# Kernel tuning notes

Measured on AMD Instinct MI355X. Metric: run time of the kernel, lower is better.

## Reference

```python
import jax, jax.numpy as jnp
import numpy as np

B, D, OUT, K = 2048, 256, 256, 16


def setup_inputs() -> dict:
    key = jax.random.key(0)
    k1, k2, k3, k4 = jax.random.split(key, 4)
    x = jax.random.normal(k1, (B, D), dtype=jnp.float32)
    values = jax.random.uniform(k2, (OUT, D, K), dtype=jnp.float32, minval=-0.05, maxval=0.05)
    skip_w = jax.random.normal(k3, (OUT, D), dtype=jnp.float32) * (1.0 / np.sqrt(D).astype(np.float32))
    skip_b = jax.random.normal(k4, (OUT,), dtype=jnp.float32) * 0.01
    return {"x": x, "values": values, "skip_w": skip_w, "skip_b": skip_b}


def reference(x, values, skip_w, skip_b):
    # x: (B, D); values: (OUT, D, K); skip_w: (OUT, D); skip_b: (OUT,)
    num_knots = values.shape[-1]
    grid = jnp.linspace(-1.0, 1.0, num_knots)  # (K,)
    xc = jnp.clip(x, -1.0, 1.0)
    # torch.bucketize(x, grid) with right=False == searchsorted side='left'
    right = jnp.searchsorted(grid, xc, side='left')
    left = jnp.clip(right - 1, 0, num_knots - 2)  # (B, D)
    right = left + 1
    g0 = grid[left]
    g1 = grid[right]
    w = (xc - g0) / (g1 - g0 + 1e-12)  # (B, D)
    # Gather spline values per (sample, input-dim) knot bucket.
    vt = jnp.transpose(values, (1, 2, 0))  # (D, K, OUT)
    dim_idx = jnp.arange(xc.shape[1])[None, :]  # (1, D)
    v_left = vt[dim_idx, left]    # (B, D, OUT)
    v_right = vt[dim_idx, right]  # (B, D, OUT)
    # Linear interpolation + sum over input dims.
    y = jnp.sum((1.0 - w)[..., None] * v_left + w[..., None] * v_right, axis=1)  # (B, OUT)
    # Skip connection on the clamped input (torch reassigns x = clamp(x) first).
    return y + xc @ skip_w.T + skip_b
```

## Files before the change

kernel.cpp:

```cpp
#include <hip/hip_runtime.h>
#include <hip/hip_bf16.h>


namespace {
constexpr int Bsz  = 2048;
constexpr int Din  = 256;
constexpr int Dout = 256;
constexpr int Kn   = 16;
constexpr int KKNOT = Din * Kn;
constexpr int KB    = KKNOT / 32;
constexpr float INV_H = 7.5f;
constexpr float Hgrid = 2.0f / 15.0f;

constexpr int NSPLIT = 8;
constexpr int STK    = 8;
constexpr int SXS    = 36;
}

typedef __attribute__((ext_vector_type(8))) short shortx8;
typedef __attribute__((ext_vector_type(4))) float floatx4;

__device__ __forceinline__ unsigned int f2bf(float f) {
  __hip_bfloat16 h = __float2bfloat16(f);
  return (unsigned int)*reinterpret_cast<unsigned short*>(&h);
}
__device__ __forceinline__ float clamp1(float v) {
  return fminf(1.f, fmaxf(-1.f, v));
}
__device__ __forceinline__ unsigned int packbf(unsigned int e0, unsigned int e1) {
  return (e1 & 0xffff0000u) | (e0 >> 16);
}
__device__ __forceinline__ unsigned int rnd(float f) {
  return __float_as_uint(f) + 0x8000u;
}

__global__ __launch_bounds__(256) void kan_prep(
    const float* __restrict__ values, const float* __restrict__ skip_w,
    unsigned short* __restrict__ Wf) {
  const int tid = blockIdx.x * 256 + threadIdx.x;
  const int q  = tid & 3;
  const int n  = (tid >> 2) & 15;
  const int og = (tid >> 6) & 15;
  const int kb = tid >> 10;
  const int o  = og * 16 + n;
  const int k0 = kb * 32 + q * 8;
  const int d  = k0 >> 4;
  const float h0 = (float)(k0 & 15);
  const float sw = skip_w[o * Din + d];
  const float* src = values + (size_t)o * KKNOT + k0;
  const float4 v0 = *(const float4*)src;
  const float4 v1 = *(const float4*)(src + 4);
  float e[8] = {v0.x, v0.y, v0.z, v0.w, v1.x, v1.y, v1.z, v1.w};
  #pragma unroll
  for (int j = 0; j < 8; ++j)
    e[j] = fmaf(-1.f + (h0 + (float)j) * Hgrid, sw, e[j]);
  const size_t chunk = (size_t)kb * 1024 + og * 64 + q * 16 + n;
  *(uint4*)(Wf + chunk * 8) = make_uint4(
      f2bf(e[0]) | (f2bf(e[1]) << 16), f2bf(e[2]) | (f2bf(e[3]) << 16),
      f2bf(e[4]) | (f2bf(e[5]) << 16), f2bf(e[6]) | (f2bf(e[7]) << 16));
}

__global__ __launch_bounds__(256) void kan_gemm(
    const float* __restrict__ x, const unsigned short* __restrict__ Wf,
    float* __restrict__ part) {
  __shared__ float sx[32 * SXS];
  __shared__ __align__(16) unsigned short aLds[2][32 * 64];

  const int tid  = threadIdx.x;
  const int wave = tid >> 6, lane = tid & 63;
  const int ks   = blockIdx.x >> 6;
  const int mi   = blockIdx.x & 63;
  const int m0   = mi * 32;
  const int og0  = wave * 4;
  const int lrow = lane & 15, lq = lane >> 4;

  const int brow = tid >> 3;
  const int bseg = tid & 7;
  const int kbi  = bseg >> 2;
  const int dsel = (bseg >> 1) & 1;
  const float h0 = (float)((bseg & 1) * 8);

  const uint4* B = (const uint4*)Wf;

  floatx4 acc[2][4] = {};
  uint4 bb[2][8];

  const int kb0 = ks * 16;
  const int d0  = ks * 32;
  {
    const float4 v = *(const float4*)(x + (size_t)(m0 + brow) * Din + d0 + bseg * 4);
    *(float4*)&sx[brow * SXS + bseg * 4] = v;
  }
  __syncthreads();

  #pragma unroll
  for (int kk = 0; kk < 2; ++kk)
    #pragma unroll
    for (int j = 0; j < 4; ++j)
      bb[0][kk * 4 + j] = B[(size_t)(kb0 + kk) * 1024 + (og0 + j) * 64 + lane];
  {
    const float xv = sx[brow * SXS + 2 * kbi + dsel];
    const float t  = (clamp1(xv) + 1.f) * INV_H;
    unsigned int e[8];
    #pragma unroll
    for (int h = 0; h < 8; ++h)
      e[h] = rnd(fmaxf(0.f, 1.f - fabsf(t - (h0 + (float)h))));
    *(uint4*)&aLds[0][brow * 64 + bseg * 8] =
        make_uint4(packbf(e[0], e[1]), packbf(e[2], e[3]),
                   packbf(e[4], e[5]), packbf(e[6], e[7]));
  }

  for (int s = 0; s < STK; ++s) {
    const int cur = s & 1, nxt = cur ^ 1;
    if (s + 1 < STK) {
      #pragma unroll
      for (int kk = 0; kk < 2; ++kk)
        #pragma unroll
        for (int j = 0; j < 4; ++j)
          bb[nxt][kk * 4 + j] =
              B[(size_t)(kb0 + 2 * (s + 1) + kk) * 1024 + (og0 + j) * 64 + lane];
    }
    __syncthreads();

    if (s + 1 < STK) {
      const float xv = sx[brow * SXS + 4 * (s + 1) + 2 * kbi + dsel];
      const float t  = (clamp1(xv) + 1.f) * INV_H;
      unsigned int e[8];
      #pragma unroll
      for (int h = 0; h < 8; ++h)
        e[h] = rnd(fmaxf(0.f, 1.f - fabsf(t - (h0 + (float)h))));
      *(uint4*)&aLds[nxt][brow * 64 + bseg * 8] =
          make_uint4(packbf(e[0], e[1]), packbf(e[2], e[3]),
                     packbf(e[4], e[5]), packbf(e[6], e[7]));
    }

    shortx8 af[2][2];
    #pragma unroll
    for (int i = 0; i < 2; ++i)
      #pragma unroll
      for (int kk = 0; kk < 2; ++kk)
        af[i][kk] = *(const shortx8*)&aLds[cur][(16 * i + lrow) * 64 + kk * 32 + lq * 8];
    #pragma unroll
    for (int kk = 0; kk < 2; ++kk)
      #pragma unroll
      for (int j = 0; j < 4; ++j) {
        union { uint4 u; shortx8 s; } bc;
        bc.u = bb[cur][kk * 4 + j];
        #pragma unroll
        for (int i = 0; i < 2; ++i)
          acc[i][j] = __builtin_amdgcn_mfma_f32_16x16x32_bf16(af[i][kk], bc.s, acc[i][j], 0, 0, 0);
      }
  }

  float4* P4 = (float4*)part;
  const size_t sbase = ((size_t)mi * NSPLIT + ks) * 2048 + wave * 512;
  #pragma unroll
  for (int i = 0; i < 2; ++i)
    #pragma unroll
    for (int j = 0; j < 4; ++j)
      P4[sbase + (i * 4 + j) * 64 + lane] =
          make_float4(acc[i][j][0], acc[i][j][1], acc[i][j][2], acc[i][j][3]);
}

__global__ __launch_bounds__(256) void kan_reduce(
    const float* __restrict__ part, const float* __restrict__ skip_b,
    float* __restrict__ out) {
  const int mi = blockIdx.x >> 3;
  const int g  = ((blockIdx.x & 7) << 8) + threadIdx.x;
  const float4* Pm = (const float4*)part + (size_t)mi * NSPLIT * 2048;
  float4 a = Pm[g];
  #pragma unroll
  for (int sp = 1; sp < NSPLIT; ++sp) {
    const float4 b = Pm[sp * 2048 + g];
    a.x += b.x; a.y += b.y; a.z += b.z; a.w += b.w;
  }
  const int w  = g >> 9, qq = g & 511;
  const int ij = qq >> 6, ln = qq & 63;
  const int i  = ij >> 2, j = ij & 3;
  const int b0 = mi * 32 + 16 * i + ((ln >> 4) << 2);
  const int o  = w * 64 + 16 * j + (ln & 15);
  const float sb = skip_b[o];
  out[(size_t)(b0 + 0) * Dout + o] = a.x + sb;
  out[(size_t)(b0 + 1) * Dout + o] = a.y + sb;
  out[(size_t)(b0 + 2) * Dout + o] = a.z + sb;
  out[(size_t)(b0 + 3) * Dout + o] = a.w + sb;
}

__device__ __forceinline__ void knot_interp(float xraw, float& xv, float& w, int& l) {
  xv = fminf(1.0f, fmaxf(-1.0f, xraw));
  float t = (xv + 1.0f) * INV_H;
  l = (int)ceilf(t) - 1;
  l = l < 0 ? 0 : (l > Kn - 2 ? Kn - 2 : l);
  float g0 = -1.0f + Hgrid * (float)l;
  w = (xv - g0) * INV_H;
}

__global__ __launch_bounds__(256) void prep_transpose(
    const float* __restrict__ values, const float* __restrict__ skip_w,
    float* __restrict__ vt, float* __restrict__ swt) {
  int idx = blockIdx.x * blockDim.x + threadIdx.x;
  if (idx < Din * Kn * Dout) {
    int k = idx & (Kn - 1);
    int d = (idx >> 4) & (Din - 1);
    int o = idx >> 12;
    vt[(d * Kn + k) * Dout + o] = values[idx];
  }
  if (idx < Dout * Din) {
    int d = idx & (Din - 1);
    int o = idx >> 8;
    swt[d * Dout + o] = skip_w[idx];
  }
}

__global__ __launch_bounds__(256) void kan_main(
    const float* __restrict__ x, const float* __restrict__ vt,
    const float* __restrict__ swt, const float* __restrict__ skip_b,
    float* __restrict__ out) {
  __shared__ float s_w[4][Din];
  __shared__ float s_x[4][Din];
  __shared__ int   s_l[4][Din];
  const int tid = threadIdx.x;
  const int b0  = blockIdx.x * 4;
  for (int i = tid; i < 4 * Din; i += 256) {
    int bb = i >> 8;
    int d  = i & (Din - 1);
    float xv, w; int l;
    knot_interp(x[(b0 + bb) * Din + d], xv, w, l);
    s_w[bb][d] = w; s_x[bb][d] = xv; s_l[bb][d] = l;
  }
  __syncthreads();
  const int g = tid >> 6, lane = tid & 63;
  const int o = lane << 2, b = b0 + g;
  float4 acc = make_float4(0.f, 0.f, 0.f, 0.f);
  for (int d = 0; d < Din; ++d) {
    const float w = s_w[g][d], xv = s_x[g][d];
    const int l = s_l[g][d];
    const float* base = vt + (d * Kn + l) * Dout + o;
    const float4 vl = *(const float4*)(base);
    const float4 vr = *(const float4*)(base + Dout);
    const float4 sw = *(const float4*)(swt + d * Dout + o);
    acc.x = fmaf(xv, sw.x, fmaf(w, vr.x - vl.x, acc.x + vl.x));
    acc.y = fmaf(xv, sw.y, fmaf(w, vr.y - vl.y, acc.y + vl.y));
    acc.z = fmaf(xv, sw.z, fmaf(w, vr.z - vl.z, acc.z + vl.z));
    acc.w = fmaf(xv, sw.w, fmaf(w, vr.w - vl.w, acc.w + vl.w));
  }
  const float4 bias = *(const float4*)(skip_b + o);
  acc.x += bias.x; acc.y += bias.y; acc.z += bias.z; acc.w += bias.w;
  *(float4*)(out + (size_t)b * Dout + o) = acc;
}

extern "C" void kernel_launch(void* const* d_in, const int* in_sizes, int n_in,
                              void* d_out, int out_size, void* d_ws, size_t ws_size,
                              hipStream_t stream) {
  (void)in_sizes; (void)n_in; (void)out_size;
  const float* x      = (const float*)d_in[0];
  const float* values = (const float*)d_in[1];
  const float* skip_w = (const float*)d_in[2];
  const float* skip_b = (const float*)d_in[3];
  float* out = (float*)d_out;

  const size_t wf_bytes   = (size_t)Dout * KKNOT * sizeof(unsigned short);
  const size_t part_bytes = (size_t)64 * NSPLIT * 8192 * sizeof(float);
  const size_t need_gemm  = wf_bytes + part_bytes;
  const size_t need_fb    = (size_t)(Din * Kn * Dout + Din * Dout) * sizeof(float);

  if (ws_size >= need_gemm) {
    unsigned short* Wf = (unsigned short*)d_ws;
    float* part        = (float*)((char*)d_ws + wf_bytes);
    kan_prep<<<(KB * 1024) / 256, 256, 0, stream>>>(values, skip_w, Wf);
    kan_gemm<<<64 * NSPLIT, 256, 0, stream>>>(x, Wf, part);
    kan_reduce<<<512, 256, 0, stream>>>(part, skip_b, out);
  } else if (ws_size >= need_fb) {
    float* vt  = (float*)d_ws;
    float* swt = vt + Din * Kn * Dout;
    prep_transpose<<<(Din * Kn * Dout + 255) / 256, 256, 0, stream>>>(values, skip_w, vt, swt);
    kan_main<<<Bsz / 4, 256, 0, stream>>>(x, vt, swt, skip_b, out);
  }
}
```

Measured before the change: 78.10 us.

## Replace split-K GEMM plus reduce with full-K GEMM tiled over output columns

Drops the split-K partitioning and the separate reduction kernel. Each block now covers 32 rows and 64 output columns over the full K range, writing results plus bias directly. An XOR swizzle is added to the A-tile LDS layout to avoid bank conflicts. The launch shrinks to 256 blocks, each with far fewer MFMAs per sync, and the A basis tile is rebuilt redundantly by each of the four output-quarter blocks. This removes the partial-sum traffic and one launch but lowers the work per block and the parallelism along K.

```diff
diff --git a/kernel.cpp b/kernel.cpp
--- a/kernel.cpp
+++ b/kernel.cpp
@@ -12,9 +12,8 @@
 constexpr float INV_H = 7.5f;
 constexpr float Hgrid = 2.0f / 15.0f;
 
-constexpr int NSPLIT = 8;
-constexpr int STK    = 8;
-constexpr int SXS    = 36;
+constexpr int NSTEP = KKNOT / 64;
+constexpr int SXS   = 260;
 }
 
 typedef __attribute__((ext_vector_type(8))) short shortx8;
@@ -32,6 +31,33 @@
 }
 __device__ __forceinline__ unsigned int rnd(float f) {
   return __float_as_uint(f) + 0x8000u;
+}
+
+__device__ __forceinline__ void buildA(unsigned short* dst, float xv, float h0) {
+  const float t = (clamp1(xv) + 1.f) * INV_H;
+  unsigned int e[8];
+  #pragma unroll
+  for (int h = 0; h < 8; ++h)
+    e[h] = rnd(fmaxf(0.f, 1.f - fabsf(t - (h0 + (float)h))));
+  *(uint4*)dst = make_uint4(packbf(e[0], e[1]), packbf(e[2], e[3]),
+                            packbf(e[4], e[5]), packbf(e[6], e[7]));
+}
+
+__device__ __forceinline__ void mstep(const unsigned short* aBuf,
+                                      const uint4 b0, const uint4 b1,
+                                      const int o00, const int o01,
+                                      const int o10, const int o11,
+                                      floatx4& acc0, floatx4& acc1) {
+  const shortx8 a00 = *(const shortx8*)(aBuf + o00);
+  const shortx8 a10 = *(const shortx8*)(aBuf + o10);
+  const shortx8 a01 = *(const shortx8*)(aBuf + o01);
+  const shortx8 a11 = *(const shortx8*)(aBuf + o11);
+  union { uint4 u; shortx8 s; } c0, c1;
+  c0.u = b0; c1.u = b1;
+  acc0 = __builtin_amdgcn_mfma_f32_16x16x32_bf16(a00, c0.s, acc0, 0, 0, 0);
+  acc1 = __builtin_amdgcn_mfma_f32_16x16x32_bf16(a10, c0.s, acc1, 0, 0, 0);
+  acc0 = __builtin_amdgcn_mfma_f32_16x16x32_bf16(a01, c1.s, acc0, 0, 0, 0);
+  acc1 = __builtin_amdgcn_mfma_f32_16x16x32_bf16(a11, c1.s, acc1, 0, 0, 0);
 }
 
 __global__ __launch_bounds__(256) void kan_prep(
@@ -60,18 +86,18 @@
       f2bf(e[4]) | (f2bf(e[5]) << 16), f2bf(e[6]) | (f2bf(e[7]) << 16));
 }
 
-__global__ __launch_bounds__(256) void kan_gemm(
+__global__ __launch_bounds__(256) void kan_gemm_full(
     const float* __restrict__ x, const unsigned short* __restrict__ Wf,
-    float* __restrict__ part) {
+    const float* __restrict__ skip_b, float* __restrict__ out) {
   __shared__ float sx[32 * SXS];
   __shared__ __align__(16) unsigned short aLds[2][32 * 64];
 
   const int tid  = threadIdx.x;
   const int wave = tid >> 6, lane = tid & 63;
-  const int ks   = blockIdx.x >> 6;
   const int mi   = blockIdx.x & 63;
+  const int oq   = blockIdx.x >> 6;
   const int m0   = mi * 32;
-  const int og0  = wave * 4;
+  const int og   = oq * 4 + wave;
   const int lrow = lane & 15, lq = lane >> 4;
 
   const int brow = tid >> 3;
@@ -80,110 +106,63 @@
   const int dsel = (bseg >> 1) & 1;
   const float h0 = (float)((bseg & 1) * 8);
 
+  const int swz   = lrow & 7;
+  const int o00   = lrow * 64 + ((lq ^ swz) << 3);
+  const int o01   = lrow * 64 + (((4 | lq) ^ swz) << 3);
+  const int o10   = o00 + 16 * 64;
+  const int o11   = o01 + 16 * 64;
+  const int awoff = brow * 64 + ((bseg ^ (brow & 7)) << 3);
+
   const uint4* B = (const uint4*)Wf;
 
-  floatx4 acc[2][4] = {};
-  uint4 bb[2][8];
-
-  const int kb0 = ks * 16;
-  const int d0  = ks * 32;
-  {
-    const float4 v = *(const float4*)(x + (size_t)(m0 + brow) * Din + d0 + bseg * 4);
-    *(float4*)&sx[brow * SXS + bseg * 4] = v;
-  }
+  floatx4 acc0 = {}, acc1 = {};
+  uint4 bb0[2], bb1[2];
+
+  for (int i = tid; i < 32 * 64; i += 256) {
+    const int r = i >> 6, c = i & 63;
+    *(float4*)&sx[r * SXS + c * 4] = *(const float4*)(x + (size_t)(m0 + r) * Din + c * 4);
+  }
+  bb0[0] = B[(size_t)0 * 1024 + og * 64 + lane];
+  bb0[1] = B[(size_t)1 * 1024 + og * 64 + lane];
+  bb1[0] = B[(size_t)2 * 1024 + og * 64 + lane];
+  bb1[1] = B[(size_t)3 * 1024 + og * 64 + lane];
   __syncthreads();
 
-  #pragma unroll
-  for (int kk = 0; kk < 2; ++kk)
-    #pragma unroll
-    for (int j = 0; j < 4; ++j)
-      bb[0][kk * 4 + j] = B[(size_t)(kb0 + kk) * 1024 + (og0 + j) * 64 + lane];
-  {
-    const float xv = sx[brow * SXS + 2 * kbi + dsel];
-    const float t  = (clamp1(xv) + 1.f) * INV_H;
-    unsigned int e[8];
-    #pragma unroll
-    for (int h = 0; h < 8; ++h)
-      e[h] = rnd(fmaxf(0.f, 1.f - fabsf(t - (h0 + (float)h))));
-    *(uint4*)&aLds[0][brow * 64 + bseg * 8] =
-        make_uint4(packbf(e[0], e[1]), packbf(e[2], e[3]),
-                   packbf(e[4], e[5]), packbf(e[6], e[7]));
-  }
-
-  for (int s = 0; s < STK; ++s) {
-    const int cur = s & 1, nxt = cur ^ 1;
-    if (s + 1 < STK) {
-      #pragma unroll
-      for (int kk = 0; kk < 2; ++kk)
-        #pragma unroll
-        for (int j = 0; j < 4; ++j)
-          bb[nxt][kk * 4 + j] =
-              B[(size_t)(kb0 + 2 * (s + 1) + kk) * 1024 + (og0 + j) * 64 + lane];
+  buildA(&aLds[0][awoff], sx[brow * SXS + 2 * kbi + dsel], h0);
+
+  for (int s = 0; s < NSTEP; s += 2) {
+    {
+      const uint4 c0 = bb0[0], c1 = bb0[1];
+      if (s + 2 < NSTEP) {
+        bb0[0] = B[(size_t)(2 * (s + 2)    ) * 1024 + og * 64 + lane];
+        bb0[1] = B[(size_t)(2 * (s + 2) + 1) * 1024 + og * 64 + lane];
+      }
+      __syncthreads();
+      buildA(&aLds[1][awoff], sx[brow * SXS + 4 * (s + 1) + 2 * kbi + dsel], h0);
+      mstep(aLds[0], c0, c1, o00, o01, o10, o11, acc0, acc1);
     }
-    __syncthreads();
-
-    if (s + 1 < STK) {
-      const float xv = sx[brow * SXS + 4 * (s + 1) + 2 * kbi + dsel];
-      const float t  = (clamp1(xv) + 1.f) * INV_H;
-      unsigned int e[8];
-      #pragma unroll
-      for (int h = 0; h < 8; ++h)
-        e[h] = rnd(fmaxf(0.f, 1.f - fabsf(t - (h0 + (float)h))));
-      *(uint4*)&aLds[nxt][brow * 64 + bseg * 8] =
-          make_uint4(packbf(e[0], e[1]), packbf(e[2], e[3]),
-                     packbf(e[4], e[5]), packbf(e[6], e[7]));
+    {
+      const uint4 c0 = bb1[0], c1 = bb1[1];
+      if (s + 3 < NSTEP) {
+        bb1[0] = B[(size_t)(2 * (s + 3)    ) * 1024 + og * 64 + lane];
+        bb1[1] = B[(size_t)(2 * (s + 3) + 1) * 1024 + og * 64 + lane];
+      }
+      __syncthreads();
+      if (s + 2 < NSTEP)
+        buildA(&aLds[0][awoff], sx[brow * SXS + 4 * (s + 2) + 2 * kbi + dsel], h0);
+      mstep(aLds[1], c0, c1, o00, o01, o10, o11, acc0, acc1);
     }
-
-    shortx8 af[2][2];
-    #pragma unroll
-    for (int i = 0; i < 2; ++i)
-      #pragma unroll
-      for (int kk = 0; kk < 2; ++kk)
-        af[i][kk] = *(const shortx8*)&aLds[cur][(16 * i + lrow) * 64 + kk * 32 + lq * 8];
-    #pragma unroll
-    for (int kk = 0; kk < 2; ++kk)
-      #pragma unroll
-      for (int j = 0; j < 4; ++j) {
-        union { uint4 u; shortx8 s; } bc;
-        bc.u = bb[cur][kk * 4 + j];
-        #pragma unroll
-        for (int i = 0; i < 2; ++i)
-          acc[i][j] = __builtin_amdgcn_mfma_f32_16x16x32_bf16(af[i][kk], bc.s, acc[i][j], 0, 0, 0);
-      }
-  }
-
-  float4* P4 = (float4*)part;
-  const size_t sbase = ((size_t)mi * NSPLIT + ks) * 2048 + wave * 512;
-  #pragma unroll
-  for (int i = 0; i < 2; ++i)
-    #pragma unroll
-    for (int j = 0; j < 4; ++j)
-      P4[sbase + (i * 4 + j) * 64 + lane] =
-          make_float4(acc[i][j][0], acc[i][j][1], acc[i][j][2], acc[i][j][3]);
-}
-
-__global__ __launch_bounds__(256) void kan_reduce(
-    const float* __restrict__ part, const float* __restrict__ skip_b,
-    float* __restrict__ out) {
-  const int mi = blockIdx.x >> 3;
-  const int g  = ((blockIdx.x & 7) << 8) + threadIdx.x;
-  const float4* Pm = (const float4*)part + (size_t)mi * NSPLIT * 2048;
-  float4 a = Pm[g];
-  #pragma unroll
-  for (int sp = 1; sp < NSPLIT; ++sp) {
-    const float4 b = Pm[sp * 2048 + g];
-    a.x += b.x; a.y += b.y; a.z += b.z; a.w += b.w;
-  }
-  const int w  = g >> 9, qq = g & 511;
-  const int ij = qq >> 6, ln = qq & 63;
-  const int i  = ij >> 2, j = ij & 3;
-  const int b0 = mi * 32 + 16 * i + ((ln >> 4) << 2);
-  const int o  = w * 64 + 16 * j + (ln & 15);
-  const float sb = skip_b[o];
-  out[(size_t)(b0 + 0) * Dout + o] = a.x + sb;
-  out[(size_t)(b0 + 1) * Dout + o] = a.y + sb;
-  out[(size_t)(b0 + 2) * Dout + o] = a.z + sb;
-  out[(size_t)(b0 + 3) * Dout + o] = a.w + sb;
+  }
+
+  const int ocol = og * 16 + lrow;
+  const int r0   = m0 + lq * 4;
+  const float sb = skip_b[ocol];
+  #pragma unroll
+  for (int j = 0; j < 4; ++j)
+    out[(size_t)(r0 + j) * Dout + ocol] = acc0[j] + sb;
+  #pragma unroll
+  for (int j = 0; j < 4; ++j)
+    out[(size_t)(r0 + 16 + j) * Dout + ocol] = acc1[j] + sb;
 }
 
 __device__ __forceinline__ void knot_interp(float xraw, float& xv, float& w, int& l) {
@@ -259,17 +238,13 @@
   const float* skip_b = (const float*)d_in[3];
   float* out = (float*)d_out;
 
-  const size_t wf_bytes   = (size_t)Dout * KKNOT * sizeof(unsigned short);
-  const size_t part_bytes = (size_t)64 * NSPLIT * 8192 * sizeof(float);
-  const size_t need_gemm  = wf_bytes + part_bytes;
-  const size_t need_fb    = (size_t)(Din * Kn * Dout + Din * Dout) * sizeof(float);
-
-  if (ws_size >= need_gemm) {
+  const size_t wf_bytes = (size_t)Dout * KKNOT * sizeof(unsigned short);
+  const size_t need_fb  = (size_t)(Din * Kn * Dout + Din * Dout) * sizeof(float);
+
+  if (ws_size >= wf_bytes) {
     unsigned short* Wf = (unsigned short*)d_ws;
-    float* part        = (float*)((char*)d_ws + wf_bytes);
     kan_prep<<<(KB * 1024) / 256, 256, 0, stream>>>(values, skip_w, Wf);
-    kan_gemm<<<64 * NSPLIT, 256, 0, stream>>>(x, Wf, part);
-    kan_reduce<<<512, 256, 0, stream>>>(part, skip_b, out);
+    kan_gemm_full<<<256, 256, 0, stream>>>(x, Wf, skip_b, out);
   } else if (ws_size >= need_fb) {
     float* vt  = (float*)d_ws;
     float* swt = vt + Din * Kn * Dout;
```

After: 88.69 us. 1.14x slower.

## Replace split-K partial buffer and reduce kernel with atomic adds into output

Applied to the files above, without the earlier changes.

The separate reduction kernel and its partial-sum workspace are removed. The prep kernel now initializes the output with the bias, and each split-K GEMM block atomically adds its accumulators straight into the output. This drops one launch and the write and read of the partial buffer, but adds 8-way float atomic contention per element and makes the summation order nondeterministic.

```diff
diff --git a/kernel.cpp b/kernel.cpp
--- a/kernel.cpp
+++ b/kernel.cpp
@@ -36,8 +36,13 @@
 
 __global__ __launch_bounds__(256) void kan_prep(
     const float* __restrict__ values, const float* __restrict__ skip_w,
-    unsigned short* __restrict__ Wf) {
+    const float* __restrict__ skip_b, unsigned short* __restrict__ Wf,
+    float* __restrict__ out) {
   const int tid = blockIdx.x * 256 + threadIdx.x;
+  {
+    const float4 sb = *(const float4*)(skip_b + ((tid << 2) & (Dout - 1)));
+    *(float4*)(out + (size_t)tid * 4) = sb;
+  }
   const int q  = tid & 3;
   const int n  = (tid >> 2) & 15;
   const int og = (tid >> 6) & 15;
@@ -62,7 +67,7 @@
 
 __global__ __launch_bounds__(256) void kan_gemm(
     const float* __restrict__ x, const unsigned short* __restrict__ Wf,
-    float* __restrict__ part) {
+    float* __restrict__ out) {
   __shared__ float sx[32 * SXS];
   __shared__ __align__(16) unsigned short aLds[2][32 * 64];
 
@@ -152,38 +157,18 @@
       }
   }
 
-  float4* P4 = (float4*)part;
-  const size_t sbase = ((size_t)mi * NSPLIT + ks) * 2048 + wave * 512;
   #pragma unroll
   for (int i = 0; i < 2; ++i)
     #pragma unroll
-    for (int j = 0; j < 4; ++j)
-      P4[sbase + (i * 4 + j) * 64 + lane] =
-          make_float4(acc[i][j][0], acc[i][j][1], acc[i][j][2], acc[i][j][3]);
-}
-
-__global__ __launch_bounds__(256) void kan_reduce(
-    const float* __restrict__ part, const float* __restrict__ skip_b,
-    float* __restrict__ out) {
-  const int mi = blockIdx.x >> 3;
-  const int g  = ((blockIdx.x & 7) << 8) + threadIdx.x;
-  const float4* Pm = (const float4*)part + (size_t)mi * NSPLIT * 2048;
-  float4 a = Pm[g];
-  #pragma unroll
-  for (int sp = 1; sp < NSPLIT; ++sp) {
-    const float4 b = Pm[sp * 2048 + g];
-    a.x += b.x; a.y += b.y; a.z += b.z; a.w += b.w;
-  }
-  const int w  = g >> 9, qq = g & 511;
-  const int ij = qq >> 6, ln = qq & 63;
-  const int i  = ij >> 2, j = ij & 3;
-  const int b0 = mi * 32 + 16 * i + ((ln >> 4) << 2);
-  const int o  = w * 64 + 16 * j + (ln & 15);
-  const float sb = skip_b[o];
-  out[(size_t)(b0 + 0) * Dout + o] = a.x + sb;
-  out[(size_t)(b0 + 1) * Dout + o] = a.y + sb;
-  out[(size_t)(b0 + 2) * Dout + o] = a.z + sb;
-  out[(size_t)(b0 + 3) * Dout + o] = a.w + sb;
+    for (int j = 0; j < 4; ++j) {
+      const int col  = (og0 + j) * 16 + lrow;
+      const int row0 = m0 + i * 16 + lq * 4;
+      float* op = out + (size_t)row0 * Dout + col;
+      atomicAdd(op,            acc[i][j][0]);
+      atomicAdd(op + Dout,     acc[i][j][1]);
+      atomicAdd(op + 2 * Dout, acc[i][j][2]);
+      atomicAdd(op + 3 * Dout, acc[i][j][3]);
+    }
 }
 
 __device__ __forceinline__ void knot_interp(float xraw, float& xv, float& w, int& l) {
@@ -259,17 +244,13 @@
   const float* skip_b = (const float*)d_in[3];
   float* out = (float*)d_out;
 
-  const size_t wf_bytes   = (size_t)Dout * KKNOT * sizeof(unsigned short);
-  const size_t part_bytes = (size_t)64 * NSPLIT * 8192 * sizeof(float);
-  const size_t need_gemm  = wf_bytes + part_bytes;
-  const size_t need_fb    = (size_t)(Din * Kn * Dout + Din * Dout) * sizeof(float);
-
-  if (ws_size >= need_gemm) {
+  const size_t wf_bytes = (size_t)Dout * KKNOT * sizeof(unsigned short);
+  const size_t need_fb  = (size_t)(Din * Kn * Dout + Din * Dout) * sizeof(float);
+
+  if (ws_size >= wf_bytes) {
     unsigned short* Wf = (unsigned short*)d_ws;
-    float* part        = (float*)((char*)d_ws + wf_bytes);
-    kan_prep<<<(KB * 1024) / 256, 256, 0, stream>>>(values, skip_w, Wf);
-    kan_gemm<<<64 * NSPLIT, 256, 0, stream>>>(x, Wf, part);
-    kan_reduce<<<512, 256, 0, stream>>>(part, skip_b, out);
+    kan_prep<<<(KB * 1024) / 256, 256, 0, stream>>>(values, skip_w, skip_b, Wf, out);
+    kan_gemm<<<64 * NSPLIT, 256, 0, stream>>>(x, Wf, out);
   } else if (ws_size >= need_fb) {
     float* vt  = (float*)d_ws;
     float* swt = vt + Din * Kn * Dout;
```

New measurement: 82.93 us. 6.2% more time.

## Fuse prep, GEMM and reduce into one cooperative kernel with grid syncs

Applied to the files above, without the earlier changes.

Merges the three launches (weight prep, split-K MFMA GEMM, partial reduction) into a single cooperative kernel of 512 blocks, separated by grid-wide barriers, so launch gaps between kernels go away. It also fully unrolls the GEMM stage loop. If the cooperative launch fails it falls back to the original three kernels. In exchange it adds two grid.sync barriers and sets launch_bounds(256,2), which constrains registers so all 512 blocks can be co-resident.

```diff
diff --git a/kernel.cpp b/kernel.cpp
--- a/kernel.cpp
+++ b/kernel.cpp
@@ -1,5 +1,8 @@
 #include <hip/hip_runtime.h>
 #include <hip/hip_bf16.h>
+#include <hip/hip_cooperative_groups.h>
+
+namespace cg = cooperative_groups;
 
 
 namespace {
@@ -34,14 +37,14 @@
   return __float_as_uint(f) + 0x8000u;
 }
 
-__global__ __launch_bounds__(256) void kan_prep(
-    const float* __restrict__ values, const float* __restrict__ skip_w,
+
+__device__ __forceinline__ void prep_body(
+    int gtid, const float* __restrict__ values, const float* __restrict__ skip_w,
     unsigned short* __restrict__ Wf) {
-  const int tid = blockIdx.x * 256 + threadIdx.x;
-  const int q  = tid & 3;
-  const int n  = (tid >> 2) & 15;
-  const int og = (tid >> 6) & 15;
-  const int kb = tid >> 10;
+  const int q  = gtid & 3;
+  const int n  = (gtid >> 2) & 15;
+  const int og = (gtid >> 6) & 15;
+  const int kb = gtid >> 10;
   const int o  = og * 16 + n;
   const int k0 = kb * 32 + q * 8;
   const int d  = k0 >> 4;
@@ -60,16 +63,13 @@
       f2bf(e[4]) | (f2bf(e[5]) << 16), f2bf(e[6]) | (f2bf(e[7]) << 16));
 }
 
-__global__ __launch_bounds__(256) void kan_gemm(
+__device__ __forceinline__ void gemm_body(
+    int bid, int tid, float* sx, unsigned short (*aLds)[32 * 64],
     const float* __restrict__ x, const unsigned short* __restrict__ Wf,
     float* __restrict__ part) {
-  __shared__ float sx[32 * SXS];
-  __shared__ __align__(16) unsigned short aLds[2][32 * 64];
-
-  const int tid  = threadIdx.x;
   const int wave = tid >> 6, lane = tid & 63;
-  const int ks   = blockIdx.x >> 6;
-  const int mi   = blockIdx.x & 63;
+  const int ks   = bid >> 6;
+  const int mi   = bid & 63;
   const int m0   = mi * 32;
   const int og0  = wave * 4;
   const int lrow = lane & 15, lq = lane >> 4;
@@ -110,6 +110,7 @@
                    packbf(e[4], e[5]), packbf(e[6], e[7]));
   }
 
+  #pragma unroll
   for (int s = 0; s < STK; ++s) {
     const int cur = s & 1, nxt = cur ^ 1;
     if (s + 1 < STK) {
@@ -162,11 +163,10 @@
           make_float4(acc[i][j][0], acc[i][j][1], acc[i][j][2], acc[i][j][3]);
 }
 
-__global__ __launch_bounds__(256) void kan_reduce(
-    const float* __restrict__ part, const float* __restrict__ skip_b,
-    float* __restrict__ out) {
-  const int mi = blockIdx.x >> 3;
-  const int g  = ((blockIdx.x & 7) << 8) + threadIdx.x;
+__device__ __forceinline__ void reduce_body(
+    int mi, int sub, int tid, const float* __restrict__ part,
+    const float* __restrict__ skip_b, float* __restrict__ out) {
+  const int g = (sub << 8) + tid;
   const float4* Pm = (const float4*)part + (size_t)mi * NSPLIT * 2048;
   float4 a = Pm[g];
   #pragma unroll
@@ -184,6 +184,47 @@
   out[(size_t)(b0 + 1) * Dout + o] = a.y + sb;
   out[(size_t)(b0 + 2) * Dout + o] = a.z + sb;
   out[(size_t)(b0 + 3) * Dout + o] = a.w + sb;
+}
+
+__global__ __launch_bounds__(256, 2) void kan_fused(
+    const float* __restrict__ x, const float* __restrict__ values,
+    const float* __restrict__ skip_w, const float* __restrict__ skip_b,
+    unsigned short* __restrict__ Wf, float* __restrict__ part,
+    float* __restrict__ out) {
+  __shared__ float sx[32 * SXS];
+  __shared__ __align__(16) unsigned short aLds[2][32 * 64];
+
+  const int tid = threadIdx.x;
+  const int bid = blockIdx.x;
+  cg::grid_group grid = cg::this_grid();
+
+  prep_body(bid * 256 + tid, values, skip_w, Wf);
+  grid.sync();
+
+  gemm_body(bid, tid, sx, aLds, x, Wf, part);
+  grid.sync();
+
+  reduce_body(bid & 63, bid >> 6, tid, part, skip_b, out);
+}
+
+__global__ __launch_bounds__(256) void kan_prep(
+    const float* __restrict__ values, const float* __restrict__ skip_w,
+    unsigned short* __restrict__ Wf) {
+  prep_body(blockIdx.x * 256 + threadIdx.x, values, skip_w, Wf);
+}
+
+__global__ __launch_bounds__(256) void kan_gemm(
+    const float* __restrict__ x, const unsigned short* __restrict__ Wf,
+    float* __restrict__ part) {
+  __shared__ float sx[32 * SXS];
+  __shared__ __align__(16) unsigned short aLds[2][32 * 64];
+  gemm_body(blockIdx.x, threadIdx.x, sx, aLds, x, Wf, part);
+}
+
+__global__ __launch_bounds__(256) void kan_reduce(
+    const float* __restrict__ part, const float* __restrict__ skip_b,
+    float* __restrict__ out) {
+  reduce_body(blockIdx.x & 63, blockIdx.x >> 6, threadIdx.x, part, skip_b, out);
 }
 
 __device__ __forceinline__ void knot_interp(float xraw, float& xv, float& w, int& l) {
@@ -267,9 +308,16 @@
   if (ws_size >= need_gemm) {
     unsigned short* Wf = (unsigned short*)d_ws;
     float* part        = (float*)((char*)d_ws + wf_bytes);
-    kan_prep<<<(KB * 1024) / 256, 256, 0, stream>>>(values, skip_w, Wf);
-    kan_gemm<<<64 * NSPLIT, 256, 0, stream>>>(x, Wf, part);
-    kan_reduce<<<512, 256, 0, stream>>>(part, skip_b, out);
+    void* args[7] = {(void*)&x, (void*)&values, (void*)&skip_w, (void*)&skip_b,
+                     (void*)&Wf, (void*)&part, (void*)&out};
+    hipError_t e = hipLaunchCooperativeKernel((const void*)kan_fused, dim3(512),
+                                              dim3(256), args, 0, stream);
+    if (e != hipSuccess) {
+      (void)hipGetLastError();
+      kan_prep<<<512, 256, 0, stream>>>(values, skip_w, Wf);
+      kan_gemm<<<512, 256, 0, stream>>>(x, Wf, part);
+      kan_reduce<<<512, 256, 0, stream>>>(part, skip_b, out);
+    }
   } else if (ws_size >= need_fb) {
     float* vt  = (float*)d_ws;
     float* swt = vt + Din * Kn * Dout;
```

After: 220.5 us. 2.82x slower.
